# Kernel optimization log

Hardware: AMD Instinct MI355X
Metric: run time of the kernel (lower is better)

The kernel has to match this reference:

```python
import jax, jax.numpy as jnp
import numpy as np

S = 7          # number of slots
B = 8192       # batch
D = 1024       # input_dim
E = 256        # slot_embedding_dim
H = 512        # rnn_hidden_dim
SH = 256       # slot_hidden_dim
V = 100        # labels per slot (uniform)


def _lstm_cell(x, h, c, W_ih, W_hh, b_ih, b_hh):
    # PyTorch LSTMCell: gates ordered i, f, g, o
    gates = x @ W_ih.T + b_ih + h @ W_hh.T + b_hh
    i, f, g, o = jnp.split(gates, 4, axis=-1)
    i = jax.nn.sigmoid(i); f = jax.nn.sigmoid(f)
    g = jnp.tanh(g); o = jax.nn.sigmoid(o)
    c_new = f * c + i * g
    h_new = o * jnp.tanh(c_new)
    return h_new, c_new


def setup_inputs() -> dict:
    key = jax.random.key(0)
    ks = jax.random.split(key, 24)
    sc = 0.05
    D0 = D + E  # layer-0 input size
    inp = {
        'inputs': jax.random.normal(ks[0], (B, D), jnp.float32),
        'labels': jax.random.randint(ks[1], (S - 1, B), 0, V),
        'start': jax.random.normal(ks[2], (E,), jnp.float32),
        'emb': jax.random.normal(ks[3], (S - 1, V, E), jnp.float32) * sc,
        # layer 0 (input size D0)
        'W_ih0': jax.random.normal(ks[4], (S, 4 * H, D0), jnp.float32) * sc,
        'W_hh0': jax.random.normal(ks[5], (S, 4 * H, H), jnp.float32) * sc,
        'b_ih0': jax.random.normal(ks[6], (S, 4 * H), jnp.float32) * sc,
        'b_hh0': jax.random.normal(ks[7], (S, 4 * H), jnp.float32) * sc,
        'hwN_W0': jax.random.normal(ks[8], (S, H, D0 + H), jnp.float32) * sc,
        'hwN_b0': jax.random.normal(ks[9], (S, H), jnp.float32) * sc,
        'hwL_W0': jax.random.normal(ks[10], (S, H, D0), jnp.float32) * sc,
        # layer 1 (input size H)
        'W_ih1': jax.random.normal(ks[11], (S, 4 * H, H), jnp.float32) * sc,
        'W_hh1': jax.random.normal(ks[12], (S, 4 * H, H), jnp.float32) * sc,
        'b_ih1': jax.random.normal(ks[13], (S, 4 * H), jnp.float32) * sc,
        'b_hh1': jax.random.normal(ks[14], (S, 4 * H), jnp.float32) * sc,
        'hwN_W1': jax.random.normal(ks[15], (S, H, H + H), jnp.float32) * sc,
        'hwN_b1': jax.random.normal(ks[16], (S, H), jnp.float32) * sc,
        'hwL_W1': jax.random.normal(ks[17], (S, H, H), jnp.float32) * sc,
        # slot hidden + classifier
        'sh_W': jax.random.normal(ks[18], (S, SH, H), jnp.float32) * sc,
        'sh_b': jax.random.normal(ks[19], (S, SH), jnp.float32) * sc,
        'pred_W': jax.random.normal(ks[20], (S, V, SH), jnp.float32) * sc,
        'pred_b': jax.random.normal(ks[21], (S, V), jnp.float32) * sc,
    }
    return inp


def reference(inputs, labels, start, emb,
              W_ih0, W_hh0, b_ih0, b_hh0, hwN_W0, hwN_b0, hwL_W0,
              W_ih1, W_hh1, b_ih1, b_hh1, hwN_W1, hwN_b1, hwL_W1,
              sh_W, sh_b, pred_W, pred_b):
    bsz = inputs.shape[0]
    cur_emb = jnp.broadcast_to(start[None, :], (bsz, E))
    h0 = jnp.zeros((bsz, H), inputs.dtype); c0 = jnp.zeros((bsz, H), inputs.dtype)
    h1 = jnp.zeros((bsz, H), inputs.dtype); c1 = jnp.zeros((bsz, H), inputs.dtype)
    logits_all = []
    for i in range(S):  # slots are a short, structurally distinct recurrence
        x = jnp.concatenate([inputs, cur_emb], axis=-1)  # [B, D+E]
        # layer 0
        h0, c0 = _lstm_cell(x, h0, c0, W_ih0[i], W_hh0[i], b_ih0[i], b_hh0[i])
        gate = jax.nn.sigmoid(jnp.concatenate([x, h0], -1) @ hwN_W0[i].T + hwN_b0[i])
        cur = gate * h0 + (1.0 - gate) * (x @ hwL_W0[i].T)
        # layer 1
        h1, c1 = _lstm_cell(cur, h1, c1, W_ih1[i], W_hh1[i], b_ih1[i], b_hh1[i])
        gate1 = jax.nn.sigmoid(jnp.concatenate([cur, h1], -1) @ hwN_W1[i].T + hwN_b1[i])
        # (highway output of last layer feeds nothing further for this slot)
        _ = gate1 * h1 + (1.0 - gate1) * (cur @ hwL_W1[i].T)
        hidden = jax.nn.relu(h1 @ sh_W[i].T + sh_b[i])     # [B, SH]
        logits_all.append(hidden @ pred_W[i].T + pred_b[i])  # [B, V]
        if i < S - 1:
            cur_emb = emb[i][labels[i]]  # teacher-forced embedding lookup
    return jnp.stack(logits_all, axis=0)  # [S, B, V]
```

## Files before the change

### kernel.cpp

```cpp
#include <hip/hip_runtime.h>

#define SLOTS 7
#define BATCH 8192

typedef __attribute__((ext_vector_type(8))) __bf16 bf16x8;
typedef __attribute__((ext_vector_type(4))) float f32x4;

__device__ __forceinline__ void gl_lds16(const __bf16* g, __bf16* l) {
  __builtin_amdgcn_global_load_lds(
      (const __attribute__((address_space(1))) void*)g,
      (__attribute__((address_space(3))) void*)l, 16, 0, 0);
}

__device__ __forceinline__ float sigmoidf_(float x) {
  return 1.f / (1.f + __expf(-x));
}
__device__ __forceinline__ float tanhf_(float x) {
  float xc = fminf(fmaxf(x, -15.f), 15.f);
  float e = __expf(2.f * xc);
  return (e - 1.f) / (e + 1.f);
}

#define VMW(n) asm volatile("s_waitcnt vmcnt(" #n ")" ::: "memory")
#define BARF()                       \
  __builtin_amdgcn_s_barrier();      \
  asm volatile("" ::: "memory")

__global__ void __launch_bounds__(512, 2)
gemm8p(const __bf16* __restrict__ A, int lda,
       const __bf16* __restrict__ Bw, int ldb,
       const float* __restrict__ b_ih, const float* __restrict__ b_hh,
       float* __restrict__ cst, __bf16* __restrict__ hout, int hld, int hoff,
       int N, int NT) {
  extern __shared__ __bf16 lds[];
#define LDSH(b, s) (lds + (((b) << 2) + (s)) * 8192)
  const int tid = threadIdx.x;
  const int w = tid >> 6, lane = tid & 63;
  const int wr = w >> 2, wc = w & 3;
  const int ln = lane & 15, lh = lane >> 4;
  const int nbx = N >> 8;
  const int NB = gridDim.x;
  const int bid = blockIdx.x;
  const int wg = (bid & 7) * (NB >> 3) + (bid >> 3);
  const int bx = wg % nbx, by = wg / nbx;
  const int blockM = by << 8, blockN = bx << 8;

  f32x4 acc[8][4];
#pragma unroll
  for (int i = 0; i < 8; ++i)
#pragma unroll
    for (int j = 0; j < 4; ++j) acc[i][j] = (f32x4){0.f, 0.f, 0.f, 0.f};

  auto stage = [&](int nb, int s, int kt) {
    const __bf16* base = (s & 1) ? Bw : A;
    const int ld = (s & 1) ? ldb : lda;
    const int rb = (s & 1) ? blockN : blockM;
    const int kh = s >> 1;
#pragma unroll
    for (int j = 0; j < 2; ++j) {
      const int c = j * 512 + w * 64 + lane;
      const int row = c >> 2;
      const int blklog = (c & 3) ^ ((c >> 3) & 3);
      const __bf16* src =
          base + (size_t)(rb + row) * ld + kt * 64 + kh * 32 + blklog * 8;
      gl_lds16(src, LDSH(nb, s) + j * 4096 + w * 512);
    }
  };

  bf16x8 a[8], b0[2], b1[2];
  const int swz = ((lh ^ ((ln >> 1) & 3)) << 3);

#define RDA(slot)                                                            \
  {                                                                          \
    const __bf16* ap = LDSH(buf, slot);                                      \
    _Pragma("unroll") for (int mi = 0; mi < 8; ++mi) a[mi] =                 \
        *(const bf16x8*)&ap[(wr * 128 + mi * 16 + ln) * 32 + swz];           \
  }
#define RDB(slot)                                                            \
  {                                                                          \
    const __bf16* bp = LDSH(buf, slot);                                      \
    _Pragma("unroll") for (int ni = 0; ni < 2; ++ni) {                       \
      b0[ni] = *(const bf16x8*)&bp[(wc * 64 + ni * 16 + ln) * 32 + swz];     \
      b1[ni] = *(const bf16x8*)&bp[(wc * 64 + 32 + ni * 16 + ln) * 32 + swz];\
    }                                                                        \
  }
#define MFMAC(bp, nh)                                                        \
  __builtin_amdgcn_s_setprio(1);                                             \
  _Pragma("unroll") for (int mi = 0; mi < 8; ++mi)                           \
      _Pragma("unroll") for (int ni = 0; ni < 2; ++ni)                       \
          acc[mi][(nh)*2 + ni] = __builtin_amdgcn_mfma_f32_16x16x32_bf16(    \
              a[mi], bp[ni], acc[mi][(nh)*2 + ni], 0, 0, 0);                 \
  __builtin_amdgcn_s_setprio(0);

#pragma unroll
  for (int s4 = 0; s4 < 4; ++s4) stage(0, s4, 0);
  VMW(0);
  BARF();

  int buf = 0;
  for (int t = 0; t < NT; ++t) {
    const int nb = buf ^ 1;
    const bool hn = (t + 1 < NT);
    if (hn) {
      stage(nb, 0, t + 1); stage(nb, 1, t + 1);
      stage(nb, 2, t + 1); stage(nb, 3, t + 1);
    }
    RDA(0); RDB(1);
    MFMAC(b0, 0); MFMAC(b1, 1);
    RDA(2); RDB(3);
    MFMAC(b0, 0); MFMAC(b1, 1);
    VMW(0);
    BARF();
    buf = nb;
  }
#undef RDA
#undef RDB
#undef MFMAC
#undef LDSH

  const int row0 = blockM + wr * 128 + (lh << 2);
  const int h = (((blockN >> 6) + wc) << 4) + ln;
  const float bs0 = b_ih[h] + b_hh[h];
  const float bs1 = b_ih[512 + h] + b_hh[512 + h];
  const float bs2 = b_ih[1024 + h] + b_hh[1024 + h];
  const float bs3 = b_ih[1536 + h] + b_hh[1536 + h];
#pragma unroll
  for (int mi = 0; mi < 8; ++mi)
#pragma unroll
    for (int r = 0; r < 4; ++r) {
      const int row = row0 + mi * 16 + r;
      float gi = sigmoidf_(acc[mi][0][r] + bs0);
      float gf = sigmoidf_(acc[mi][1][r] + bs1);
      float gg = tanhf_(acc[mi][2][r] + bs2);
      float go = sigmoidf_(acc[mi][3][r] + bs3);
      const size_t ci = (size_t)row * 512 + h;
      float cn = gf * cst[ci] + gi * gg;
      cst[ci] = cn;
      hout[(size_t)row * hld + hoff + h] = (__bf16)(go * tanhf_(cn));
    }
}

template <int MODE>
__global__ void __launch_bounds__(256)
gemm_bt(const __bf16* __restrict__ A, int lda,
        const __bf16* __restrict__ Bw, int ldb,
        void* __restrict__ Cout, int ldc,
        const float* __restrict__ bias,
        const float* __restrict__ auxr,
        __bf16* __restrict__ hout, int hld, int hoff,
        const __bf16* __restrict__ hsrc,
        int M, int N, int K, int Nreal) {
  __shared__ __align__(16) __bf16 As[2][128 * 32];
  __shared__ __align__(16) __bf16 Bs[2][128 * 32];
  const int w = threadIdx.x >> 6;
  const int lane = threadIdx.x & 63;
  const int wr = w >> 1, wc = w & 1;
  const int rowBase = blockIdx.y << 7;
  const int colBase = blockIdx.x << 7;
  const int sr = lane >> 2;
  const int sc = (lane & 3) << 3;

  f32x4 acc[4][4];
#pragma unroll
  for (int i = 0; i < 4; ++i)
#pragma unroll
    for (int j = 0; j < 4; ++j) acc[i][j] = (f32x4){0.f, 0.f, 0.f, 0.f};

  const int nsteps = K >> 5;

#define STAGE(bi, k0)                                                           \
  {                                                                             \
    const __bf16* ga = A + (size_t)(rowBase + (w << 5) + sr) * lda + (k0) + sc; \
    gl_lds16(ga, &As[(bi)][(w << 5) * 32]);                                     \
    gl_lds16(ga + (size_t)16 * lda, &As[(bi)][((w << 5) + 16) * 32]);           \
    const __bf16* gb = Bw + (size_t)(colBase + (w << 5) + sr) * ldb + (k0) + sc;\
    gl_lds16(gb, &Bs[(bi)][(w << 5) * 32]);                                     \
    gl_lds16(gb + (size_t)16 * ldb, &Bs[(bi)][((w << 5) + 16) * 32]);           \
  }

  STAGE(0, 0);
  __syncthreads();
  int buf = 0;
  const int ln = lane & 15;
  const int kg = (lane >> 4) << 3;
  for (int t = 0; t < nsteps; ++t) {
    if (t + 1 < nsteps) STAGE(buf ^ 1, (t + 1) << 5);
    bf16x8 av[4], bv[4];
#pragma unroll
    for (int i = 0; i < 4; ++i)
      av[i] = *(const bf16x8*)&As[buf][((wr << 6) + (i << 4) + ln) * 32 + kg];
#pragma unroll
    for (int i = 0; i < 4; ++i)
      bv[i] = *(const bf16x8*)&Bs[buf][((wc << 6) + (i << 4) + ln) * 32 + kg];
#pragma unroll
    for (int mi = 0; mi < 4; ++mi)
#pragma unroll
      for (int ni = 0; ni < 4; ++ni)
        acc[mi][ni] = __builtin_amdgcn_mfma_f32_16x16x32_bf16(
            av[mi], bv[ni], acc[mi][ni], 0, 0, 0);
    __syncthreads();
    buf ^= 1;
  }
#undef STAGE

  const int lh = lane >> 4;
  const int row0 = rowBase + (wr << 6) + (lh << 2);
  const int col0 = colBase + (wc << 6) + ln;

  if (MODE == 0) {
    float* C = (float*)Cout;
#pragma unroll
    for (int mi = 0; mi < 4; ++mi)
#pragma unroll
      for (int ni = 0; ni < 4; ++ni) {
        const int col = col0 + (ni << 4);
#pragma unroll
        for (int r = 0; r < 4; ++r)
          C[(size_t)(row0 + (mi << 4) + r) * ldc + col] = acc[mi][ni][r];
      }
  } else if (MODE == 1) {
    __bf16* C = (__bf16*)Cout;
#pragma unroll
    for (int mi = 0; mi < 4; ++mi)
#pragma unroll
      for (int ni = 0; ni < 4; ++ni) {
        const int col = col0 + (ni << 4);
        const float b = bias[col];
#pragma unroll
        for (int r = 0; r < 4; ++r) {
          float v = fmaxf(acc[mi][ni][r] + b, 0.f);
          C[(size_t)(row0 + (mi << 4) + r) * ldc + col] = (__bf16)v;
        }
      }
  } else if (MODE == 2) {
    float* C = (float*)Cout;
#pragma unroll
    for (int mi = 0; mi < 4; ++mi)
#pragma unroll
      for (int ni = 0; ni < 4; ++ni) {
        const int col = col0 + (ni << 4);
        if (col < Nreal) {
          const float b = bias[col];
#pragma unroll
          for (int r = 0; r < 4; ++r)
            C[(size_t)(row0 + (mi << 4) + r) * ldc + col] = acc[mi][ni][r] + b;
        }
      }
  } else if (MODE == 6) {
    __bf16* C = (__bf16*)Cout;
#pragma unroll
    for (int mi = 0; mi < 4; ++mi)
#pragma unroll
      for (int ni = 0; ni < 4; ++ni) {
        const int col = col0 + (ni << 4);
#pragma unroll
        for (int r = 0; r < 4; ++r) {
          const int row = row0 + (mi << 4) + r;
          float xp = auxr[(size_t)row * 1024 + col];
          float hwl = auxr[(size_t)row * 1024 + 512 + col];
          float gn = sigmoidf_(acc[mi][ni][r] + xp + bias[col]);
          float hn = (float)hsrc[(size_t)row * 512 + col];
          C[(size_t)row * ldc + col] = (__bf16)(gn * hn + (1.f - gn) * hwl);
          hout[(size_t)row * hld + hoff + col] = (__bf16)hn;
        }
      }
  }
}

#define PR0 2621440
#define PR1 3670016
#define PR2 4325376
#define PR3 4980736
#define PR4 5242880
#define PR5 6291456
#define PR6 7340032
#define PR7 7471104
#define PR8 7503872
__global__ void pack_all(const float* __restrict__ W_ih0, const float* __restrict__ W_hh0,
                         const float* __restrict__ hwN_W0, const float* __restrict__ hwL_W0,
                         const float* __restrict__ W_ih1, const float* __restrict__ W_hh1,
                         const float* __restrict__ sh_W, const float* __restrict__ pred_W,
                         __bf16* __restrict__ WA, __bf16* __restrict__ WX,
                         __bf16* __restrict__ WH, __bf16* __restrict__ WB,
                         __bf16* __restrict__ WS, __bf16* __restrict__ WP, int s) {
  const int idx = blockIdx.x * 256 + threadIdx.x;
  if (idx >= PR8) return;
  if (idx < PR0) {
    int i = idx, r = i / 1280, c = i - r * 1280;
    int sr = (((r >> 4) & 3) << 9) + ((r >> 6) << 4) + (r & 15);
    WA[(long)r * 1792 + c] = (__bf16)W_ih0[(size_t)s * 2048 * 1280 + (long)sr * 1280 + c];
  } else if (idx < PR1) {
    int i = idx - PR0, r = i >> 9, c = i & 511;
    int sr = (((r >> 4) & 3) << 9) + ((r >> 6) << 4) + (r & 15);
    WA[(long)r * 1792 + 1280 + c] = (__bf16)W_hh0[(size_t)s * 2048 * 512 + (long)sr * 512 + c];
  } else if (idx < PR2) {
    int i = idx - PR1, r = i / 1280, c = i - r * 1280;
    WX[(long)r * 1280 + c] = (__bf16)hwN_W0[(size_t)s * 512 * 1792 + (long)r * 1792 + c];
  } else if (idx < PR3) {
    int i = idx - PR2, r = i / 1280, c = i - r * 1280;
    WX[(long)(512 + r) * 1280 + c] = (__bf16)hwL_W0[(size_t)s * 512 * 1280 + (long)r * 1280 + c];
  } else if (idx < PR4) {
    int i = idx - PR3, r = i >> 9, c = i & 511;
    WH[(long)r * 512 + c] = (__bf16)hwN_W0[(size_t)s * 512 * 1792 + (long)r * 1792 + 1280 + c];
  } else if (idx < PR5) {
    int i = idx - PR4, r = i >> 9, c = i & 511;
    int sr = (((r >> 4) & 3) << 9) + ((r >> 6) << 4) + (r & 15);
    WB[(long)r * 1024 + c] = (__bf16)W_ih1[(size_t)s * 2048 * 512 + (long)sr * 512 + c];
  } else if (idx < PR6) {
    int i = idx - PR5, r = i >> 9, c = i & 511;
    int sr = (((r >> 4) & 3) << 9) + ((r >> 6) << 4) + (r & 15);
    WB[(long)r * 1024 + 512 + c] = (__bf16)W_hh1[(size_t)s * 2048 * 512 + (long)sr * 512 + c];
  } else if (idx < PR7) {
    int i = idx - PR6, r = i >> 9, c = i & 511;
    WS[(long)r * 512 + c] = (__bf16)sh_W[(size_t)s * 256 * 512 + (long)r * 512 + c];
  } else {
    int i = idx - PR7, r = i >> 8, c = i & 255;
    float v = (r < 100) ? pred_W[(size_t)s * 100 * 256 + (long)r * 256 + c] : 0.f;
    WP[(long)r * 256 + c] = (__bf16)v;
  }
}

__global__ void conv_inputs(const float* __restrict__ in, __bf16* __restrict__ xh) {
  int idx = blockIdx.x * 256 + threadIdx.x;
  int b = idx >> 10, c = idx & 1023;
  xh[(size_t)b * 1792 + c] = (__bf16)in[idx];
}

__global__ void set_start(const float* __restrict__ start, __bf16* __restrict__ xh) {
  int idx = blockIdx.x * 256 + threadIdx.x;
  int b = idx >> 8, e = idx & 255;
  xh[(size_t)b * 1792 + 1024 + e] = (__bf16)start[e];
}

__global__ void emb_gather(const float* __restrict__ emb, const int* __restrict__ labels,
                           __bf16* __restrict__ xh) {
  int idx = blockIdx.x * 256 + threadIdx.x;
  int b = idx >> 8, e = idx & 255;
  int lab = labels[b];
  xh[(size_t)b * 1792 + 1024 + e] = (__bf16)emb[(size_t)lab * 256 + e];
}

__global__ void zero_states(__bf16* __restrict__ xh, __bf16* __restrict__ xh1A) {
  int idx = blockIdx.x * 256 + threadIdx.x;
  int b = idx >> 9, h = idx & 511;
  xh[(size_t)b * 1792 + 1280 + h] = (__bf16)0.f;
  xh1A[(size_t)b * 1024 + 512 + h] = (__bf16)0.f;
}

extern "C" void kernel_launch(void* const* d_in, const int* in_sizes, int n_in,
                              void* d_out, int out_size, void* d_ws, size_t ws_size,
                              hipStream_t stream) {
  const float* inputs = (const float*)d_in[0];
  const int* labels = (const int*)d_in[1];
  const float* start = (const float*)d_in[2];
  const float* emb = (const float*)d_in[3];
  const float* W_ih0 = (const float*)d_in[4];
  const float* W_hh0 = (const float*)d_in[5];
  const float* b_ih0 = (const float*)d_in[6];
  const float* b_hh0 = (const float*)d_in[7];
  const float* hwN_W0 = (const float*)d_in[8];
  const float* hwN_b0 = (const float*)d_in[9];
  const float* hwL_W0 = (const float*)d_in[10];
  const float* W_ih1 = (const float*)d_in[11];
  const float* W_hh1 = (const float*)d_in[12];
  const float* b_ih1 = (const float*)d_in[13];
  const float* b_hh1 = (const float*)d_in[14];
  const float* sh_W = (const float*)d_in[18];
  const float* sh_b = (const float*)d_in[19];
  const float* pred_W = (const float*)d_in[20];
  const float* pred_b = (const float*)d_in[21];
  float* out = (float*)d_out;

  char* p = (char*)d_ws;
  size_t off = 0;
  auto alloc = [&](size_t bytes) {
    void* r = p + off;
    off += (bytes + 255) & ~(size_t)255;
    return r;
  };
  __bf16* WA = (__bf16*)alloc((size_t)2048 * 1792 * 2);
  __bf16* WX = (__bf16*)alloc((size_t)1024 * 1280 * 2);
  __bf16* WH = (__bf16*)alloc((size_t)512 * 512 * 2);
  __bf16* WB = (__bf16*)alloc((size_t)2048 * 1024 * 2);
  __bf16* WS = (__bf16*)alloc((size_t)256 * 512 * 2);
  __bf16* WP = (__bf16*)alloc((size_t)128 * 256 * 2);
  __bf16* xh = (__bf16*)alloc((size_t)BATCH * 1792 * 2);
  __bf16* xh1A = (__bf16*)alloc((size_t)BATCH * 1024 * 2);
  __bf16* xh1B = (__bf16*)alloc((size_t)BATCH * 1024 * 2);
  __bf16* h0new = (__bf16*)alloc((size_t)BATCH * 512 * 2);
  float* ghw = (float*)alloc((size_t)BATCH * 1024 * 4);
  float* c0 = (float*)alloc((size_t)BATCH * 512 * 4);
  float* c1 = (float*)alloc((size_t)BATCH * 512 * 4);
  __bf16* hidden = (__bf16*)ghw;
  (void)ws_size; (void)in_sizes; (void)n_in; (void)out_size;

  hipMemsetAsync(c0, 0, (size_t)BATCH * 512 * 4, stream);
  hipMemsetAsync(c1, 0, (size_t)BATCH * 512 * 4, stream);
  zero_states<<<BATCH * 512 / 256, 256, 0, stream>>>(xh, xh1A);
  conv_inputs<<<BATCH * 1024 / 256, 256, 0, stream>>>(inputs, xh);
  set_start<<<BATCH * 256 / 256, 256, 0, stream>>>(start, xh);

  const dim3 blk(256);
  for (int s = 0; s < SLOTS; ++s) {
    __bf16* xcur = (s & 1) ? xh1B : xh1A;
    __bf16* xnext = (s & 1) ? xh1A : xh1B;
    pack_all<<<(PR8 + 255) / 256, blk, 0, stream>>>(
        W_ih0, W_hh0, hwN_W0, hwL_W0, W_ih1, W_hh1, sh_W, pred_W,
        WA, WX, WH, WB, WS, WP, s);

    gemm_bt<0><<<dim3(8, 64), blk, 0, stream>>>(
        xh, 1792, WX, 1280, ghw, 1024, nullptr,
        nullptr, nullptr, 0, 0, nullptr, BATCH, 1024, 1280, 1024);
    gemm8p<<<256, 512, 131072, stream>>>(
        xh, 1792, WA, 1792, b_ih0 + s * 2048, b_hh0 + s * 2048,
        c0, h0new, 512, 0, 2048, 28);
    gemm_bt<6><<<dim3(4, 64), blk, 0, stream>>>(
        h0new, 512, WH, 512, xcur, 1024, hwN_b0 + s * 512,
        ghw, xh, 1792, 1280, h0new, BATCH, 512, 512, 512);
    if (s < SLOTS - 1)
      emb_gather<<<BATCH * 256 / 256, blk, 0, stream>>>(
          emb + (size_t)s * 100 * 256, labels + (size_t)s * BATCH, xh);
    gemm8p<<<256, 512, 131072, stream>>>(
        xcur, 1024, WB, 1024, b_ih1 + s * 2048, b_hh1 + s * 2048,
        c1, xnext, 1024, 512, 2048, 16);
    gemm_bt<1><<<dim3(2, 64), blk, 0, stream>>>(
        xnext + 512, 1024, WS, 512, hidden, 256, sh_b + s * 256,
        nullptr, nullptr, 0, 0, nullptr, BATCH, 256, 512, 256);
    gemm_bt<2><<<dim3(1, 64), blk, 0, stream>>>(
        hidden, 256, WP, 256, out + (size_t)s * BATCH * 100, 100,
        pred_b + s * 100, nullptr, nullptr, 0, 0, nullptr, BATCH, 128, 256, 100);
  }
}
```

Before: 1.540 ms.

## Replace 256x256 LSTM gate GEMM with smaller 128x128 tiled kernel

Swaps the 512-thread 256x256-tile LSTM GEMM, which used 128KB of LDS and a BK of 64, for a 256-thread 128x128-tile kernel with BK 32 and static double-buffered LDS. The LSTM cell epilogue is kept. The smaller tiles give more blocks (1024 instead of 256) and allow higher occupancy. In exchange, each loaded element is reused less, more global and LDS traffic is needed per FLOP, and the kernel syncs more often across the K loop.

After: 1.695 ms. 10.1% more time.

```diff
diff --git a/kernel.cpp b/kernel.cpp
--- a/kernel.cpp
+++ b/kernel.cpp
@@ -21,114 +21,77 @@
   return (e - 1.f) / (e + 1.f);
 }
 
-#define VMW(n) asm volatile("s_waitcnt vmcnt(" #n ")" ::: "memory")
-#define BARF()                       \
-  __builtin_amdgcn_s_barrier();      \
-  asm volatile("" ::: "memory")
-
-__global__ void __launch_bounds__(512, 2)
-gemm8p(const __bf16* __restrict__ A, int lda,
-       const __bf16* __restrict__ Bw, int ldb,
-       const float* __restrict__ b_ih, const float* __restrict__ b_hh,
-       float* __restrict__ cst, __bf16* __restrict__ hout, int hld, int hoff,
-       int N, int NT) {
-  extern __shared__ __bf16 lds[];
-#define LDSH(b, s) (lds + (((b) << 2) + (s)) * 8192)
-  const int tid = threadIdx.x;
-  const int w = tid >> 6, lane = tid & 63;
-  const int wr = w >> 2, wc = w & 3;
-  const int ln = lane & 15, lh = lane >> 4;
-  const int nbx = N >> 8;
-  const int NB = gridDim.x;
-  const int bid = blockIdx.x;
-  const int wg = (bid & 7) * (NB >> 3) + (bid >> 3);
-  const int bx = wg % nbx, by = wg / nbx;
-  const int blockM = by << 8, blockN = bx << 8;
-
-  f32x4 acc[8][4];
-#pragma unroll
-  for (int i = 0; i < 8; ++i)
+__global__ void __launch_bounds__(256, 4)
+gemm_lstm(const __bf16* __restrict__ A, int lda,
+          const __bf16* __restrict__ Bw, int ldb,
+          const float* __restrict__ b_ih, const float* __restrict__ b_hh,
+          float* __restrict__ cst, __bf16* __restrict__ hout, int hld, int hoff,
+          int K) {
+  __shared__ __align__(16) __bf16 As[2][128 * 32];
+  __shared__ __align__(16) __bf16 Bs[2][128 * 32];
+  const int w = threadIdx.x >> 6;
+  const int lane = threadIdx.x & 63;
+  const int wr = w >> 1, wc = w & 1;
+  const int rowBase = blockIdx.y << 7;
+  const int colBase = blockIdx.x << 7;
+  const int sr = lane >> 2;
+  const int scs = (((lane & 3) ^ ((sr >> 1) & 3)) << 3);
+
+  f32x4 acc[4][4];
+#pragma unroll
+  for (int i = 0; i < 4; ++i)
 #pragma unroll
     for (int j = 0; j < 4; ++j) acc[i][j] = (f32x4){0.f, 0.f, 0.f, 0.f};
 
-  auto stage = [&](int nb, int s, int kt) {
-    const __bf16* base = (s & 1) ? Bw : A;
-    const int ld = (s & 1) ? ldb : lda;
-    const int rb = (s & 1) ? blockN : blockM;
-    const int kh = s >> 1;
-#pragma unroll
-    for (int j = 0; j < 2; ++j) {
-      const int c = j * 512 + w * 64 + lane;
-      const int row = c >> 2;
-      const int blklog = (c & 3) ^ ((c >> 3) & 3);
-      const __bf16* src =
-          base + (size_t)(rb + row) * ld + kt * 64 + kh * 32 + blklog * 8;
-      gl_lds16(src, LDSH(nb, s) + j * 4096 + w * 512);
-    }
-  };
-
-  bf16x8 a[8], b0[2], b1[2];
+  const int nsteps = K >> 5;
+
+#define STAGE(bi, k0)                                                            \
+  {                                                                              \
+    const __bf16* ga = A + (size_t)(rowBase + (w << 5) + sr) * lda + (k0) + scs; \
+    gl_lds16(ga, &As[(bi)][(w << 5) * 32]);                                      \
+    gl_lds16(ga + (size_t)16 * lda, &As[(bi)][((w << 5) + 16) * 32]);            \
+    const __bf16* gb = Bw + (size_t)(colBase + (w << 5) + sr) * ldb + (k0) + scs;\
+    gl_lds16(gb, &Bs[(bi)][(w << 5) * 32]);                                      \
+    gl_lds16(gb + (size_t)16 * ldb, &Bs[(bi)][((w << 5) + 16) * 32]);            \
+  }
+
+  STAGE(0, 0);
+  __syncthreads();
+  int buf = 0;
+  const int ln = lane & 15;
+  const int lh = lane >> 4;
   const int swz = ((lh ^ ((ln >> 1) & 3)) << 3);
-
-#define RDA(slot)                                                            \
-  {                                                                          \
-    const __bf16* ap = LDSH(buf, slot);                                      \
-    _Pragma("unroll") for (int mi = 0; mi < 8; ++mi) a[mi] =                 \
-        *(const bf16x8*)&ap[(wr * 128 + mi * 16 + ln) * 32 + swz];           \
-  }
-#define RDB(slot)                                                            \
-  {                                                                          \
-    const __bf16* bp = LDSH(buf, slot);                                      \
-    _Pragma("unroll") for (int ni = 0; ni < 2; ++ni) {                       \
-      b0[ni] = *(const bf16x8*)&bp[(wc * 64 + ni * 16 + ln) * 32 + swz];     \
-      b1[ni] = *(const bf16x8*)&bp[(wc * 64 + 32 + ni * 16 + ln) * 32 + swz];\
-    }                                                                        \
-  }
-#define MFMAC(bp, nh)                                                        \
-  __builtin_amdgcn_s_setprio(1);                                             \
-  _Pragma("unroll") for (int mi = 0; mi < 8; ++mi)                           \
-      _Pragma("unroll") for (int ni = 0; ni < 2; ++ni)                       \
-          acc[mi][(nh)*2 + ni] = __builtin_amdgcn_mfma_f32_16x16x32_bf16(    \
-              a[mi], bp[ni], acc[mi][(nh)*2 + ni], 0, 0, 0);                 \
-  __builtin_amdgcn_s_setprio(0);
-
-#pragma unroll
-  for (int s4 = 0; s4 < 4; ++s4) stage(0, s4, 0);
-  VMW(0);
-  BARF();
-
-  int buf = 0;
-  for (int t = 0; t < NT; ++t) {
-    const int nb = buf ^ 1;
-    const bool hn = (t + 1 < NT);
-    if (hn) {
-      stage(nb, 0, t + 1); stage(nb, 1, t + 1);
-      stage(nb, 2, t + 1); stage(nb, 3, t + 1);
-    }
-    RDA(0); RDB(1);
-    MFMAC(b0, 0); MFMAC(b1, 1);
-    RDA(2); RDB(3);
-    MFMAC(b0, 0); MFMAC(b1, 1);
-    VMW(0);
-    BARF();
-    buf = nb;
-  }
-#undef RDA
-#undef RDB
-#undef MFMAC
-#undef LDSH
-
-  const int row0 = blockM + wr * 128 + (lh << 2);
-  const int h = (((blockN >> 6) + wc) << 4) + ln;
+  for (int t = 0; t < nsteps; ++t) {
+    if (t + 1 < nsteps) STAGE(buf ^ 1, (t + 1) << 5);
+    bf16x8 av[4], bv[4];
+#pragma unroll
+    for (int i = 0; i < 4; ++i)
+      av[i] = *(const bf16x8*)&As[buf][((wr << 6) + (i << 4) + ln) * 32 + swz];
+#pragma unroll
+    for (int i = 0; i < 4; ++i)
+      bv[i] = *(const bf16x8*)&Bs[buf][((wc << 6) + (i << 4) + ln) * 32 + swz];
+#pragma unroll
+    for (int mi = 0; mi < 4; ++mi)
+#pragma unroll
+      for (int ni = 0; ni < 4; ++ni)
+        acc[mi][ni] = __builtin_amdgcn_mfma_f32_16x16x32_bf16(
+            av[mi], bv[ni], acc[mi][ni], 0, 0, 0);
+    __syncthreads();
+    buf ^= 1;
+  }
+#undef STAGE
+
+  const int row0 = rowBase + (wr << 6) + (lh << 2);
+  const int h = (((colBase >> 6) + wc) << 4) + ln;
   const float bs0 = b_ih[h] + b_hh[h];
   const float bs1 = b_ih[512 + h] + b_hh[512 + h];
   const float bs2 = b_ih[1024 + h] + b_hh[1024 + h];
   const float bs3 = b_ih[1536 + h] + b_hh[1536 + h];
 #pragma unroll
-  for (int mi = 0; mi < 8; ++mi)
+  for (int mi = 0; mi < 4; ++mi)
 #pragma unroll
     for (int r = 0; r < 4; ++r) {
-      const int row = row0 + mi * 16 + r;
+      const int row = row0 + (mi << 4) + r;
       float gi = sigmoidf_(acc[mi][0][r] + bs0);
       float gf = sigmoidf_(acc[mi][1][r] + bs1);
       float gg = tanhf_(acc[mi][2][r] + bs2);
@@ -411,18 +374,18 @@
     gemm_bt<0><<<dim3(8, 64), blk, 0, stream>>>(
         xh, 1792, WX, 1280, ghw, 1024, nullptr,
         nullptr, nullptr, 0, 0, nullptr, BATCH, 1024, 1280, 1024);
-    gemm8p<<<256, 512, 131072, stream>>>(
+    gemm_lstm<<<dim3(16, 64), blk, 0, stream>>>(
         xh, 1792, WA, 1792, b_ih0 + s * 2048, b_hh0 + s * 2048,
-        c0, h0new, 512, 0, 2048, 28);
+        c0, h0new, 512, 0, 1792);
     gemm_bt<6><<<dim3(4, 64), blk, 0, stream>>>(
         h0new, 512, WH, 512, xcur, 1024, hwN_b0 + s * 512,
         ghw, xh, 1792, 1280, h0new, BATCH, 512, 512, 512);
     if (s < SLOTS - 1)
       emb_gather<<<BATCH * 256 / 256, blk, 0, stream>>>(
           emb + (size_t)s * 100 * 256, labels + (size_t)s * BATCH, xh);
-    gemm8p<<<256, 512, 131072, stream>>>(
+    gemm_lstm<<<dim3(16, 64), blk, 0, stream>>>(
         xcur, 1024, WB, 1024, b_ih1 + s * 2048, b_hh1 + s * 2048,
-        c1, xnext, 1024, 512, 2048, 16);
+        c1, xnext, 1024, 512, 1024);
     gemm_bt<1><<<dim3(2, 64), blk, 0, stream>>>(
         xnext + 512, 1024, WS, 512, hidden, 256, sh_b + s * 256,
         nullptr, nullptr, 0, 0, nullptr, BATCH, 256, 512, 256);
```
